# Performance work log

Hardware: AMD Instinct MI355X
Metric: run time of the kernel (lower is better)

Reference implementation:

```python
import jax, jax.numpy as jnp
import numpy as np

MARGIN = 0.3
EPS = 1e-8


def setup_inputs() -> dict:
    key = jax.random.key(0)
    k1, k2 = jax.random.split(key)
    B, D, NUM_IDS = 8192, 128, 1024
    embeddings = jax.random.normal(k1, (B, D), dtype=jnp.float32)
    labels = jax.random.randint(k2, (B,), 0, NUM_IDS, dtype=jnp.int64)
    return {"embeddings": embeddings, "labels": labels}


def _pairwise_distance(embeddings):
    # dist[i,j] = sqrt(relu(||e_i||^2 - 2 e_i.e_j + ||e_j||^2) + eps)
    dot = embeddings @ embeddings.T                       # [B, B]
    sq = jnp.diagonal(dot)                                # [B]
    d2 = sq[None, :] - 2.0 * dot + sq[:, None]
    return jnp.sqrt(jax.nn.relu(d2) + EPS)


def reference(embeddings, labels):
    B = labels.shape[0]
    dist = _pairwise_distance(embeddings)                 # [B, B]

    same = labels[:, None] == labels[None, :]             # [B, B]
    eye = jnp.eye(B, dtype=bool)
    pos_mask = same & ~eye
    neg_mask = ~same

    neg_inf = jnp.finfo(dist.dtype).min
    pos_inf = jnp.finfo(dist.dtype).max
    hardest_pos = jnp.max(jnp.where(pos_mask, dist, neg_inf), axis=1)  # [B]
    hardest_neg = jnp.min(jnp.where(neg_mask, dist, pos_inf), axis=1)  # [B]

    valid = pos_mask.any(axis=1) & neg_mask.any(axis=1)   # [B]
    per_anchor = jax.nn.relu(hardest_pos - hardest_neg + MARGIN)
    loss_sum = jnp.sum(jnp.where(valid, per_anchor, 0.0))
    n_triplets = jnp.sum(valid)
    return loss_sum / jnp.maximum(n_triplets, 1).astype(loss_sum.dtype)
```

## Files before the change

### kernel.cpp

```cpp
#include <hip/hip_runtime.h>

#define BSZ 8192
#define DIM 128
#define NLAB 1024
#define MARGIN 0.3f
#define EPS 1e-8f
#define NJ 32
#define JCHUNK 256
#define NPH 8

typedef __bf16 bf16x8 __attribute__((ext_vector_type(8)));
typedef float f32x4 __attribute__((ext_vector_type(4)));

#define AS1 __attribute__((address_space(1)))
#define AS3 __attribute__((address_space(3)))

__device__ __forceinline__ unsigned enc_ord(float f) {
    unsigned u = __float_as_uint(f);
    return (u & 0x80000000u) ? ~u : (u | 0x80000000u);
}
__device__ __forceinline__ float dec_ord(unsigned e) {
    unsigned u = (e & 0x80000000u) ? (e & 0x7FFFFFFFu) : ~e;
    return __uint_as_float(u);
}

template <int N>
__device__ __forceinline__ void waitv() {
    if constexpr (N == 4) asm volatile("s_waitcnt vmcnt(4)" ::: "memory");
    else if constexpr (N == 2) asm volatile("s_waitcnt vmcnt(2)" ::: "memory");
    else asm volatile("s_waitcnt vmcnt(0)" ::: "memory");
}

__global__ __launch_bounds__(1024) void k_histscan(const int* __restrict__ labels,
                                                   unsigned* __restrict__ start,
                                                   unsigned* __restrict__ offset,
                                                   unsigned* __restrict__ ticket,
                                                   float* __restrict__ sumcnt) {
    __shared__ unsigned h[NLAB];
    const int tid = threadIdx.x;
    h[tid] = 0u;
    __syncthreads();
    const int4* l4 = (const int4*)labels;
    int4 a = l4[tid];
    int4 b = l4[tid + 1024];
    atomicAdd(&h[a.x], 1u); atomicAdd(&h[a.y], 1u);
    atomicAdd(&h[a.z], 1u); atomicAdd(&h[a.w], 1u);
    atomicAdd(&h[b.x], 1u); atomicAdd(&h[b.y], 1u);
    atomicAdd(&h[b.z], 1u); atomicAdd(&h[b.w], 1u);
    __syncthreads();
    for (int d = 1; d < NLAB; d <<= 1) {
        unsigned w = (tid >= d) ? h[tid - d] : 0u;
        __syncthreads();
        h[tid] += w;
        __syncthreads();
    }
    start[tid + 1] = h[tid];
    offset[tid] = (tid > 0) ? h[tid - 1] : 0u;
    if (tid == 0) {
        start[0] = 0u;
        ticket[0] = 0u;
        sumcnt[0] = 0.0f;
        ((unsigned*)sumcnt)[1] = 0u;
    }
}

__global__ __launch_bounds__(256) void k_gather(const float* __restrict__ emb,
                                                const int* __restrict__ labels,
                                                unsigned* __restrict__ offset,
                                                __bf16* __restrict__ hi,
                                                float* __restrict__ sq,
                                                int* __restrict__ slab,
                                                unsigned* __restrict__ maxp,
                                                unsigned* __restrict__ minn) {
    int row = blockIdx.x * 4 + (threadIdx.x >> 6);
    int lane = threadIdx.x & 63;
    int lab = labels[row];
    unsigned pos = 0;
    if (lane == 0) pos = atomicAdd(&offset[lab], 1u);
    pos = __shfl(pos, 0);
    float2 v = *(const float2*)&emb[(size_t)row * DIM + lane * 2];
    union { __bf16 b[2]; unsigned u; } p;
    p.b[0] = (__bf16)v.x;
    p.b[1] = (__bf16)v.y;
    ((unsigned*)hi)[pos * 64 + lane] = p.u;
    float s = v.x * v.x + v.y * v.y;
#pragma unroll
    for (int m = 32; m >= 1; m >>= 1) s += __shfl_xor(s, m);
    if (lane == 0) {
        sq[pos] = s;
        slab[pos] = lab;
        maxp[pos] = 0u;
        minn[pos] = 0xFFFFFFFFu;
    }
}

__global__ __launch_bounds__(256, 4) void k_mfma(const __bf16* __restrict__ hi,
                                                 const int* __restrict__ slab,
                                                 const unsigned* __restrict__ startp,
                                                 const float* __restrict__ sq,
                                                 unsigned* __restrict__ maxp,
                                                 unsigned* __restrict__ minn) {
    __shared__ char Bst[4][8][1024];
    __shared__ float sqlds[JCHUNK];
    __shared__ int lablds[JCHUNK];

    const int tid = threadIdx.x;
    const int lane = tid & 63;
    const int wave = tid >> 6;
    const int lr = lane & 15;
    const int lq = lane >> 4;
    const int i0 = blockIdx.x * 128;
    const int it0 = i0 + wave * 32;
    const int it1 = it0 + 16;
    const int j0 = blockIdx.y * JCHUNK;
    const float INF = __uint_as_float(0x7F800000u);

    const int lf = slab[i0];
    const int ll = slab[i0 + 127];
    const int blo = (int)startp[lf];
    const int bhi = (int)startp[ll + 1];
    unsigned mmask = 0;
#pragma unroll
    for (int tt = 0; tt < NPH; ++tt) {
        int c0 = j0 + tt * 32;
        if (bhi > c0 && blo < c0 + 32) mmask |= (1u << tt);
    }

    sqlds[tid] = sq[j0 + tid];
    lablds[tid] = slab[j0 + tid];

    bf16x8 a0[4], a1[4];
    const __bf16* ap = hi + (size_t)(it0 + lr) * DIM + lq * 8;
#pragma unroll
    for (int f = 0; f < 4; ++f) {
        a0[f] = *(const bf16x8*)&ap[f * 32];
        a1[f] = *(const bf16x8*)&ap[16 * DIM + f * 32];
        asm volatile("" : "+v"(a0[f]));
        asm volatile("" : "+v"(a1[f]));
    }
    const int4 li0 = *(const int4*)&slab[it0 + lq * 4];
    const int4 li1 = *(const int4*)&slab[it1 + lq * 4];
    const int labi0[4] = {li0.x, li0.y, li0.z, li0.w};
    const int labi1[4] = {li1.x, li1.y, li1.z, li1.w};

    float mp0[4], mp1[4], mn0[4], mn1[4];
#pragma unroll
    for (int r = 0; r < 4; ++r) {
        mp0[r] = -INF; mp1[r] = -INF;
        mn0[r] = INF;  mn1[r] = INF;
    }

    const int m0 = wave * 2, m1 = m0 + 1;
    const __bf16* bsA = hi + (size_t)(j0 + (m0 >> 2) * 16 + lr) * DIM + (m0 & 3) * 32 + lq * 8;
    const __bf16* bsB = hi + (size_t)(j0 + (m1 >> 2) * 16 + lr) * DIM + (m1 & 3) * 32 + lq * 8;
#define STAGE(t, buf)                                                              \
    do {                                                                           \
        __builtin_amdgcn_global_load_lds(                                          \
            (const AS1 void*)(bsA + (size_t)(t) * 32 * DIM),                       \
            (AS3 void*)&Bst[buf][m0][0], 16, 0, 0);                                \
        __builtin_amdgcn_global_load_lds(                                          \
            (const AS1 void*)(bsB + (size_t)(t) * 32 * DIM),                       \
            (AS3 void*)&Bst[buf][m1][0], 16, 0, 0);                                \
    } while (0)

    STAGE(0, 0);
    STAGE(1, 1);
    __syncthreads();

#pragma unroll 1
    for (int t = 0; t < NPH; ++t) {
        if (t + 2 < NPH) STAGE(t + 2, (t + 2) & 3);
        if (t < NPH - 2) waitv<4>();
        else if (t == NPH - 2) waitv<2>();
        else waitv<0>();
        __builtin_amdgcn_s_barrier();
        __builtin_amdgcn_sched_barrier(0);

        const float sqj0 = sqlds[t * 32 + lr];
        const float sqj1 = sqlds[t * 32 + 16 + lr];

        const bf16x8* bp = (const bf16x8*)&Bst[t & 3][0][0];
        f32x4 acc00 = {0, 0, 0, 0}, acc01 = {0, 0, 0, 0};
        f32x4 acc10 = {0, 0, 0, 0}, acc11 = {0, 0, 0, 0};
#pragma unroll
        for (int f = 0; f < 4; ++f) {
            bf16x8 b0 = bp[f * 64 + lane];
            bf16x8 b1 = bp[(4 + f) * 64 + lane];
            acc00 = __builtin_amdgcn_mfma_f32_16x16x32_bf16(a0[f], b0, acc00, 0, 0, 0);
            acc10 = __builtin_amdgcn_mfma_f32_16x16x32_bf16(a1[f], b0, acc10, 0, 0, 0);
            acc01 = __builtin_amdgcn_mfma_f32_16x16x32_bf16(a0[f], b1, acc01, 0, 0, 0);
            acc11 = __builtin_amdgcn_mfma_f32_16x16x32_bf16(a1[f], b1, acc11, 0, 0, 0);
        }

        if (mmask & (1u << t)) {
            const int labj0 = lablds[t * 32 + lr];
            const int labj1 = lablds[t * 32 + 16 + lr];
#pragma unroll
            for (int r = 0; r < 4; ++r) {
                float k00 = fmaf(-2.0f, acc00[r], sqj0);
                float k01 = fmaf(-2.0f, acc01[r], sqj1);
                float k10 = fmaf(-2.0f, acc10[r], sqj0);
                float k11 = fmaf(-2.0f, acc11[r], sqj1);
                bool s00 = (labj0 == labi0[r]);
                bool s01 = (labj1 == labi0[r]);
                bool s10 = (labj0 == labi1[r]);
                bool s11 = (labj1 == labi1[r]);
                mp0[r] = s00 ? fmaxf(mp0[r], k00) : mp0[r];
                mn0[r] = s00 ? mn0[r] : fminf(mn0[r], k00);
                mp0[r] = s01 ? fmaxf(mp0[r], k01) : mp0[r];
                mn0[r] = s01 ? mn0[r] : fminf(mn0[r], k01);
                mp1[r] = s10 ? fmaxf(mp1[r], k10) : mp1[r];
                mn1[r] = s10 ? mn1[r] : fminf(mn1[r], k10);
                mp1[r] = s11 ? fmaxf(mp1[r], k11) : mp1[r];
                mn1[r] = s11 ? mn1[r] : fminf(mn1[r], k11);
            }
        } else {
#pragma unroll
            for (int r = 0; r < 4; ++r) {
                float k00 = fmaf(-2.0f, acc00[r], sqj0);
                float k01 = fmaf(-2.0f, acc01[r], sqj1);
                float k10 = fmaf(-2.0f, acc10[r], sqj0);
                float k11 = fmaf(-2.0f, acc11[r], sqj1);
                mn0[r] = fminf(fminf(mn0[r], k00), k01);
                mn1[r] = fminf(fminf(mn1[r], k10), k11);
            }
        }
    }
#undef STAGE

#pragma unroll
    for (int m = 1; m < 16; m <<= 1) {
#pragma unroll
        for (int r = 0; r < 4; ++r) {
            mp0[r] = fmaxf(mp0[r], __shfl_xor(mp0[r], m));
            mn0[r] = fminf(mn0[r], __shfl_xor(mn0[r], m));
            mp1[r] = fmaxf(mp1[r], __shfl_xor(mp1[r], m));
            mn1[r] = fminf(mn1[r], __shfl_xor(mn1[r], m));
        }
    }
    if (lr == 0) {
#pragma unroll
        for (int r = 0; r < 4; ++r) {
            atomicMax(&maxp[it0 + lq * 4 + r], enc_ord(mp0[r]));
            atomicMin(&minn[it0 + lq * 4 + r], enc_ord(mn0[r]));
            atomicMax(&maxp[it1 + lq * 4 + r], enc_ord(mp1[r]));
            atomicMin(&minn[it1 + lq * 4 + r], enc_ord(mn1[r]));
        }
    }
}

__global__ __launch_bounds__(256) void k_final(const unsigned* __restrict__ maxp,
                                               const unsigned* __restrict__ minn,
                                               const float* __restrict__ sq,
                                               float* __restrict__ sumcnt,
                                               unsigned* __restrict__ ticket,
                                               float* __restrict__ out) {
    int i = blockIdx.x * 256 + threadIdx.x;
    float mpd = dec_ord(maxp[i]);
    float mnd = dec_ord(minn[i]);
    float sqi = sq[i];
    bool valid = (mpd > -1e30f) && (mnd < 1e30f);
    float hp = sqrtf(fmaxf(sqi + mpd, 0.0f) + EPS);
    float hn = sqrtf(fmaxf(sqi + mnd, 0.0f) + EPS);
    float per = valid ? fmaxf(hp - hn + MARGIN, 0.0f) : 0.0f;
    unsigned cnt = valid ? 1u : 0u;
#pragma unroll
    for (int m = 32; m >= 1; m >>= 1) {
        per += __shfl_xor(per, m);
        cnt += __shfl_xor(cnt, m);
    }
    __shared__ float ssum[4];
    __shared__ unsigned scnt[4];
    int wid = threadIdx.x >> 6;
    if ((threadIdx.x & 63) == 0) { ssum[wid] = per; scnt[wid] = cnt; }
    __syncthreads();
    if (threadIdx.x == 0) {
        float s = ssum[0] + ssum[1] + ssum[2] + ssum[3];
        unsigned c = scnt[0] + scnt[1] + scnt[2] + scnt[3];
        atomicAdd(&sumcnt[0], s);
        atomicAdd((unsigned*)&sumcnt[1], c);
        __threadfence();
        unsigned done = atomicAdd(ticket, 1u);
        if (done == gridDim.x - 1) {
            float ts = atomicAdd(&sumcnt[0], 0.0f);
            unsigned tc = atomicAdd((unsigned*)&sumcnt[1], 0u);
            out[0] = ts / (float)(tc > 0u ? tc : 1u);
        }
    }
}

extern "C" void kernel_launch(void* const* d_in, const int* in_sizes, int n_in,
                              void* d_out, int out_size, void* d_ws, size_t ws_size,
                              hipStream_t stream) {
    const float* emb    = (const float*)d_in[0];
    const int*   labels = (const int*)d_in[1];

    float* wsf = (float*)d_ws;
    __bf16*   hi     = (__bf16*)wsf;
    float*    sq     = wsf + 524288;
    unsigned* maxp   = (unsigned*)(wsf + 532480);
    unsigned* minn   = (unsigned*)(wsf + 540672);
    float*    sumcnt = wsf + 548864;
    unsigned* start  = (unsigned*)(wsf + 548868);
    unsigned* offset = (unsigned*)(wsf + 549896);
    unsigned* ticket = (unsigned*)(wsf + 550920);
    int*      slab   = (int*)(wsf + 550924);
    float*    out    = (float*)d_out;

    k_histscan<<<dim3(1), dim3(1024), 0, stream>>>(labels, start, offset, ticket, sumcnt);
    k_gather<<<dim3(BSZ / 4), dim3(256), 0, stream>>>(emb, labels, offset, hi, sq, slab, maxp, minn);
    k_mfma<<<dim3(BSZ / 128, NJ), dim3(256), 0, stream>>>(hi, slab, start, sq, maxp, minn);
    k_final<<<dim3(BSZ / 256), dim3(256), 0, stream>>>(maxp, minn, sq, sumcnt, ticket, out);
}
```

Measured before the change: 51.42 us.

## Move hardest-positive search to final kernel using sorted label ranges

```diff
diff --git a/kernel.cpp b/kernel.cpp
--- a/kernel.cpp
+++ b/kernel.cpp
@@ -26,8 +26,7 @@
 
 template <int N>
 __device__ __forceinline__ void waitv() {
-    if constexpr (N == 4) asm volatile("s_waitcnt vmcnt(4)" ::: "memory");
-    else if constexpr (N == 2) asm volatile("s_waitcnt vmcnt(2)" ::: "memory");
+    if constexpr (N == 2) asm volatile("s_waitcnt vmcnt(2)" ::: "memory");
     else asm volatile("s_waitcnt vmcnt(0)" ::: "memory");
 }
 
@@ -70,7 +69,6 @@
                                                 __bf16* __restrict__ hi,
                                                 float* __restrict__ sq,
                                                 int* __restrict__ slab,
-                                                unsigned* __restrict__ maxp,
                                                 unsigned* __restrict__ minn) {
     int row = blockIdx.x * 4 + (threadIdx.x >> 6);
     int lane = threadIdx.x & 63;
@@ -89,20 +87,17 @@
     if (lane == 0) {
         sq[pos] = s;
         slab[pos] = lab;
-        maxp[pos] = 0u;
         minn[pos] = 0xFFFFFFFFu;
     }
 }
 
-__global__ __launch_bounds__(256, 4) void k_mfma(const __bf16* __restrict__ hi,
+__global__ __launch_bounds__(256, 5) void k_mfma(const __bf16* __restrict__ hi,
                                                  const int* __restrict__ slab,
                                                  const unsigned* __restrict__ startp,
                                                  const float* __restrict__ sq,
-                                                 unsigned* __restrict__ maxp,
                                                  unsigned* __restrict__ minn) {
-    __shared__ char Bst[4][8][1024];
+    __shared__ char Bst[3][8][1024];
     __shared__ float sqlds[JCHUNK];
-    __shared__ int lablds[JCHUNK];
 
     const int tid = threadIdx.x;
     const int lane = tid & 63;
@@ -111,7 +106,6 @@
     const int lq = lane >> 4;
     const int i0 = blockIdx.x * 128;
     const int it0 = i0 + wave * 32;
-    const int it1 = it0 + 16;
     const int j0 = blockIdx.y * JCHUNK;
     const float INF = __uint_as_float(0x7F800000u);
 
@@ -127,7 +121,6 @@
     }
 
     sqlds[tid] = sq[j0 + tid];
-    lablds[tid] = slab[j0 + tid];
 
     bf16x8 a0[4], a1[4];
     const __bf16* ap = hi + (size_t)(it0 + lr) * DIM + lq * 8;
@@ -138,17 +131,22 @@
         asm volatile("" : "+v"(a0[f]));
         asm volatile("" : "+v"(a1[f]));
     }
-    const int4 li0 = *(const int4*)&slab[it0 + lq * 4];
-    const int4 li1 = *(const int4*)&slab[it1 + lq * 4];
-    const int labi0[4] = {li0.x, li0.y, li0.z, li0.w};
-    const int labi1[4] = {li1.x, li1.y, li1.z, li1.w};
-
-    float mp0[4], mp1[4], mn0[4], mn1[4];
-#pragma unroll
-    for (int r = 0; r < 4; ++r) {
-        mp0[r] = -INF; mp1[r] = -INF;
-        mn0[r] = INF;  mn1[r] = INF;
-    }
+
+    int s0i[2][4], s1i[2][4];
+#pragma unroll
+    for (int it = 0; it < 2; ++it)
+#pragma unroll
+        for (int r = 0; r < 4; ++r) {
+            int li = slab[it0 + it * 16 + lq * 4 + r];
+            s0i[it][r] = (int)startp[li];
+            s1i[it][r] = (int)startp[li + 1];
+        }
+
+    float mn[2][4];
+#pragma unroll
+    for (int it = 0; it < 2; ++it)
+#pragma unroll
+        for (int r = 0; r < 4; ++r) mn[it][r] = INF;
 
     const int m0 = wave * 2, m1 = m0 + 1;
     const __bf16* bsA = hi + (size_t)(j0 + (m0 >> 2) * 16 + lr) * DIM + (m0 & 3) * 32 + lq * 8;
@@ -169,17 +167,16 @@
 
 #pragma unroll 1
     for (int t = 0; t < NPH; ++t) {
-        if (t + 2 < NPH) STAGE(t + 2, (t + 2) & 3);
-        if (t < NPH - 2) waitv<4>();
-        else if (t == NPH - 2) waitv<2>();
+        if (t < NPH - 1) waitv<2>();
         else waitv<0>();
         __builtin_amdgcn_s_barrier();
         __builtin_amdgcn_sched_barrier(0);
+        if (t + 2 < NPH) STAGE(t + 2, (t + 2) % 3);
 
         const float sqj0 = sqlds[t * 32 + lr];
         const float sqj1 = sqlds[t * 32 + 16 + lr];
 
-        const bf16x8* bp = (const bf16x8*)&Bst[t & 3][0][0];
+        const bf16x8* bp = (const bf16x8*)&Bst[t % 3][0][0];
         f32x4 acc00 = {0, 0, 0, 0}, acc01 = {0, 0, 0, 0};
         f32x4 acc10 = {0, 0, 0, 0}, acc11 = {0, 0, 0, 0};
 #pragma unroll
@@ -193,26 +190,22 @@
         }
 
         if (mmask & (1u << t)) {
-            const int labj0 = lablds[t * 32 + lr];
-            const int labj1 = lablds[t * 32 + 16 + lr];
+            const int jj0 = j0 + t * 32 + lr;
+            const int jj1 = jj0 + 16;
 #pragma unroll
             for (int r = 0; r < 4; ++r) {
                 float k00 = fmaf(-2.0f, acc00[r], sqj0);
                 float k01 = fmaf(-2.0f, acc01[r], sqj1);
                 float k10 = fmaf(-2.0f, acc10[r], sqj0);
                 float k11 = fmaf(-2.0f, acc11[r], sqj1);
-                bool s00 = (labj0 == labi0[r]);
-                bool s01 = (labj1 == labi0[r]);
-                bool s10 = (labj0 == labi1[r]);
-                bool s11 = (labj1 == labi1[r]);
-                mp0[r] = s00 ? fmaxf(mp0[r], k00) : mp0[r];
-                mn0[r] = s00 ? mn0[r] : fminf(mn0[r], k00);
-                mp0[r] = s01 ? fmaxf(mp0[r], k01) : mp0[r];
-                mn0[r] = s01 ? mn0[r] : fminf(mn0[r], k01);
-                mp1[r] = s10 ? fmaxf(mp1[r], k10) : mp1[r];
-                mn1[r] = s10 ? mn1[r] : fminf(mn1[r], k10);
-                mp1[r] = s11 ? fmaxf(mp1[r], k11) : mp1[r];
-                mn1[r] = s11 ? mn1[r] : fminf(mn1[r], k11);
+                bool o00 = (jj0 < s0i[0][r]) || (jj0 >= s1i[0][r]);
+                bool o01 = (jj1 < s0i[0][r]) || (jj1 >= s1i[0][r]);
+                bool o10 = (jj0 < s0i[1][r]) || (jj0 >= s1i[1][r]);
+                bool o11 = (jj1 < s0i[1][r]) || (jj1 >= s1i[1][r]);
+                mn[0][r] = o00 ? fminf(mn[0][r], k00) : mn[0][r];
+                mn[0][r] = o01 ? fminf(mn[0][r], k01) : mn[0][r];
+                mn[1][r] = o10 ? fminf(mn[1][r], k10) : mn[1][r];
+                mn[1][r] = o11 ? fminf(mn[1][r], k11) : mn[1][r];
             }
         } else {
 #pragma unroll
@@ -221,58 +214,70 @@
                 float k01 = fmaf(-2.0f, acc01[r], sqj1);
                 float k10 = fmaf(-2.0f, acc10[r], sqj0);
                 float k11 = fmaf(-2.0f, acc11[r], sqj1);
-                mn0[r] = fminf(fminf(mn0[r], k00), k01);
-                mn1[r] = fminf(fminf(mn1[r], k10), k11);
+                mn[0][r] = fminf(mn[0][r], fminf(k00, k01));
+                mn[1][r] = fminf(mn[1][r], fminf(k10, k11));
             }
         }
     }
 #undef STAGE
 
 #pragma unroll
-    for (int m = 1; m < 16; m <<= 1) {
-#pragma unroll
-        for (int r = 0; r < 4; ++r) {
-            mp0[r] = fmaxf(mp0[r], __shfl_xor(mp0[r], m));
-            mn0[r] = fminf(mn0[r], __shfl_xor(mn0[r], m));
-            mp1[r] = fmaxf(mp1[r], __shfl_xor(mp1[r], m));
-            mn1[r] = fminf(mn1[r], __shfl_xor(mn1[r], m));
-        }
-    }
+    for (int m = 1; m < 16; m <<= 1)
+#pragma unroll
+        for (int it = 0; it < 2; ++it)
+#pragma unroll
+            for (int r = 0; r < 4; ++r)
+                mn[it][r] = fminf(mn[it][r], __shfl_xor(mn[it][r], m));
     if (lr == 0) {
 #pragma unroll
-        for (int r = 0; r < 4; ++r) {
-            atomicMax(&maxp[it0 + lq * 4 + r], enc_ord(mp0[r]));
-            atomicMin(&minn[it0 + lq * 4 + r], enc_ord(mn0[r]));
-            atomicMax(&maxp[it1 + lq * 4 + r], enc_ord(mp1[r]));
-            atomicMin(&minn[it1 + lq * 4 + r], enc_ord(mn1[r]));
-        }
-    }
-}
-
-__global__ __launch_bounds__(256) void k_final(const unsigned* __restrict__ maxp,
+        for (int it = 0; it < 2; ++it)
+#pragma unroll
+            for (int r = 0; r < 4; ++r)
+                atomicMin(&minn[it0 + it * 16 + lq * 4 + r], enc_ord(mn[it][r]));
+    }
+}
+
+__global__ __launch_bounds__(256) void k_final(const __bf16* __restrict__ hi,
+                                               const int* __restrict__ slab,
+                                               const unsigned* __restrict__ startp,
+                                               const float* __restrict__ sq,
                                                const unsigned* __restrict__ minn,
-                                               const float* __restrict__ sq,
                                                float* __restrict__ sumcnt,
                                                unsigned* __restrict__ ticket,
                                                float* __restrict__ out) {
-    int i = blockIdx.x * 256 + threadIdx.x;
-    float mpd = dec_ord(maxp[i]);
-    float mnd = dec_ord(minn[i]);
+    const int wave = threadIdx.x >> 6;
+    const int lane = threadIdx.x & 63;
+    const int i = blockIdx.x * 4 + wave;
+    const int lab = slab[i];
+    const int s0 = (int)startp[lab];
+    const int s1 = (int)startp[lab + 1];
+    const unsigned* h32 = (const unsigned*)hi;
+    unsigned ua = h32[(size_t)i * 64 + lane];
+    float a0 = __uint_as_float(ua << 16);
+    float a1 = __uint_as_float(ua & 0xFFFF0000u);
     float sqi = sq[i];
-    bool valid = (mpd > -1e30f) && (mnd < 1e30f);
-    float hp = sqrtf(fmaxf(sqi + mpd, 0.0f) + EPS);
-    float hn = sqrtf(fmaxf(sqi + mnd, 0.0f) + EPS);
+    float mp2 = -__uint_as_float(0x7F800000u);
+    for (int j = s0; j < s1; ++j) {
+        if (j == i) continue;
+        unsigned ub = h32[(size_t)j * 64 + lane];
+        float b0 = __uint_as_float(ub << 16);
+        float b1 = __uint_as_float(ub & 0xFFFF0000u);
+        float p = fmaf(a0, b0, a1 * b1);
+#pragma unroll
+        for (int m = 32; m >= 1; m >>= 1) p += __shfl_xor(p, m);
+        float d2 = fmaf(-2.0f, p, sqi + sq[j]);
+        mp2 = fmaxf(mp2, d2);
+    }
+    unsigned mnk = minn[i];
+    float d2n = sqi + dec_ord(mnk);
+    bool valid = ((s1 - s0) > 1) && (mnk != 0xFFFFFFFFu);
+    float hp = sqrtf(fmaxf(mp2, 0.0f) + EPS);
+    float hn = sqrtf(fmaxf(d2n, 0.0f) + EPS);
     float per = valid ? fmaxf(hp - hn + MARGIN, 0.0f) : 0.0f;
-    unsigned cnt = valid ? 1u : 0u;
-#pragma unroll
-    for (int m = 32; m >= 1; m >>= 1) {
-        per += __shfl_xor(per, m);
-        cnt += __shfl_xor(cnt, m);
-    }
+
     __shared__ float ssum[4];
     __shared__ unsigned scnt[4];
-    int wid = threadIdx.x >> 6;
-    if ((threadIdx.x & 63) == 0) { ssum[wid] = per; scnt[wid] = cnt; }
+    if (lane == 0) { ssum[wave] = per; scnt[wave] = valid ? 1u : 0u; }
     __syncthreads();
     if (threadIdx.x == 0) {
         float s = ssum[0] + ssum[1] + ssum[2] + ssum[3];
@@ -298,17 +303,16 @@
     float* wsf = (float*)d_ws;
     __bf16*   hi     = (__bf16*)wsf;
     float*    sq     = wsf + 524288;
-    unsigned* maxp   = (unsigned*)(wsf + 532480);
-    unsigned* minn   = (unsigned*)(wsf + 540672);
-    float*    sumcnt = wsf + 548864;
-    unsigned* start  = (unsigned*)(wsf + 548868);
-    unsigned* offset = (unsigned*)(wsf + 549896);
-    unsigned* ticket = (unsigned*)(wsf + 550920);
-    int*      slab   = (int*)(wsf + 550924);
+    unsigned* minn   = (unsigned*)(wsf + 532480);
+    float*    sumcnt = wsf + 540672;
+    unsigned* start  = (unsigned*)(wsf + 540676);
+    unsigned* offset = (unsigned*)(wsf + 541704);
+    unsigned* ticket = (unsigned*)(wsf + 542728);
+    int*      slab   = (int*)(wsf + 542732);
     float*    out    = (float*)d_out;
 
     k_histscan<<<dim3(1), dim3(1024), 0, stream>>>(labels, start, offset, ticket, sumcnt);
-    k_gather<<<dim3(BSZ / 4), dim3(256), 0, stream>>>(emb, labels, offset, hi, sq, slab, maxp, minn);
-    k_mfma<<<dim3(BSZ / 128, NJ), dim3(256), 0, stream>>>(hi, slab, start, sq, maxp, minn);
-    k_final<<<dim3(BSZ / 256), dim3(256), 0, stream>>>(maxp, minn, sq, sumcnt, ticket, out);
-}
+    k_gather<<<dim3(BSZ / 4), dim3(256), 0, stream>>>(emb, labels, offset, hi, sq, slab, minn);
+    k_mfma<<<dim3(BSZ / 128, NJ), dim3(256), 0, stream>>>(hi, slab, start, sq, minn);
+    k_final<<<dim3(BSZ / 4), dim3(256), 0, stream>>>(hi, slab, start, sq, minn, sumcnt, ticket, out);
+}
```

Result: slower. 114.7 us (+123.0%).
